# Optimization experiments

Measured on AMD Instinct MI355X. Metric: run time of the kernel, lower is better.

The kernel has to match this reference:

```python
import jax, jax.numpy as jnp
import numpy as np

P = 10      # num_prototypes == embed_dim
H = 2       # num_heads
F = 64      # ffn_dim
L = 2       # transformer_blocks
DH = P // H # head dim = 5


def _layernorm(x, g, b, eps=1e-5):
    mu = jnp.mean(x, axis=-1, keepdims=True)
    var = jnp.var(x, axis=-1, keepdims=True)
    return (x - mu) * jax.lax.rsqrt(var + eps) * g + b


def setup_inputs() -> dict:
    key = jax.random.key(0)
    ks = jax.random.split(key, 16)
    B = 1_000_000
    inp = {
        "x": jax.random.normal(ks[0], (B, 8), dtype=jnp.float32),
        "prototypes": jax.random.normal(ks[1], (P, 8), dtype=jnp.float32),
        # attention projections, stacked over layers
        "Wq": jax.random.normal(ks[2], (L, P, P), dtype=jnp.float32) * 0.1,
        "bq": jnp.zeros((L, P), dtype=jnp.float32),
        "Wk": jax.random.normal(ks[3], (L, P, P), dtype=jnp.float32) * 0.1,
        "bk": jnp.zeros((L, P), dtype=jnp.float32),
        "Wv": jax.random.normal(ks[4], (L, P, P), dtype=jnp.float32) * 0.1,
        "bv": jnp.zeros((L, P), dtype=jnp.float32),
        "Wo": jax.random.normal(ks[5], (L, P, P), dtype=jnp.float32) * 0.1,
        "bo": jnp.zeros((L, P), dtype=jnp.float32),
        "ln1_g": jnp.ones((L, P), dtype=jnp.float32),
        "ln1_b": jnp.zeros((L, P), dtype=jnp.float32),
        "ln2_g": jnp.ones((L, P), dtype=jnp.float32),
        "ln2_b": jnp.zeros((L, P), dtype=jnp.float32),
        # FFN
        "W1": jax.random.normal(ks[6], (L, P, F), dtype=jnp.float32) * 0.1,
        "b1": jnp.zeros((L, F), dtype=jnp.float32),
        "W2": jax.random.normal(ks[7], (L, F, P), dtype=jnp.float32) * 0.1,
        "b2": jnp.zeros((L, P), dtype=jnp.float32),
        # classifier (num_classes=2 -> single logit + sigmoid)
        "Wc": jax.random.normal(ks[8], (P, 1), dtype=jnp.float32) * 0.1,
        "bc": jnp.zeros((1,), dtype=jnp.float32),
    }
    return inp


def _forward(x, prototypes, Wq, bq, Wk, bk, Wv, bv, Wo, bo,
             ln1_g, ln1_b, ln2_g, ln2_b, W1, b1, W2, b2, Wc, bc):
    # ---- vectorized RBF kernel matrix (replaces the B*P python loop) ----
    x2 = jnp.sum(x * x, axis=-1, keepdims=True)            # [B,1]
    p2 = jnp.sum(prototypes * prototypes, axis=-1)          # [P]
    sq = x2 + p2[None, :] - 2.0 * (x @ prototypes.T)        # [B,P]
    km = jnp.exp(-sq)                                       # [B,P] quantum-kernel proxy

    seq = km[:, None, :]                                    # [B, S=1, P]
    scale = 1.0 / jnp.sqrt(jnp.asarray(DH, dtype=seq.dtype))
    B = seq.shape[0]

    for l in range(L):  # small fixed layer count
        # pre-norm multi-head self-attention (seq_len == 1)
        h = _layernorm(seq, ln1_g[l], ln1_b[l])
        q = (h @ Wq[l] + bq[l]).reshape(B, 1, H, DH)
        k = (h @ Wk[l] + bk[l]).reshape(B, 1, H, DH)
        v = (h @ Wv[l] + bv[l]).reshape(B, 1, H, DH)
        scores = jnp.einsum('bqhd,bkhd->bhqk', q, k) * scale
        attn = jax.nn.softmax(scores, axis=-1)
        o = jnp.einsum('bhqk,bkhd->bqhd', attn, v).reshape(B, 1, P)
        seq = seq + (o @ Wo[l] + bo[l])
        # pre-norm FFN
        h2 = _layernorm(seq, ln2_g[l], ln2_b[l])
        seq = seq + (jax.nn.gelu(h2 @ W1[l] + b1[l]) @ W2[l] + b2[l])

    logits = seq[:, 0, :] @ Wc + bc                          # [B,1]
    return jax.nn.sigmoid(logits)


def reference(x, prototypes, Wq, bq, Wk, bk, Wv, bv, Wo, bo,
              ln1_g, ln1_b, ln2_g, ln2_b, W1, b1, W2, b2, Wc, bc):
    return _forward(x, prototypes, Wq, bq, Wk, bk, Wv, bv, Wo, bo,
                    ln1_g, ln1_b, ln2_g, ln2_b, W1, b1, W2, b2, Wc, bc)
```

## Files before the change

kernel.cpp:

```cpp
#include <hip/hip_runtime.h>
#include <cmath>

#define PP 10
#define FF 64
#define BLOCK 256
#define NG 8
#define EPB ((BLOCK / 64) * NG * 16)
#define L2E 1.44269504088896f

typedef float f32x4 __attribute__((ext_vector_type(4)));
typedef _Float16 f16x4 __attribute__((ext_vector_type(4)));
typedef _Float16 h2 __attribute__((ext_vector_type(2)));

struct GeluCoef { float c[5]; };

#define NFRAG 19
#define FB_B2 (NFRAG * 128)
#define F_HC  (FB_B2 + 256)

__device__ __forceinline__ float fast_sigmoid(float z) {
    return __builtin_amdgcn_rcpf(1.0f + exp2f(-L2E * z));
}

__device__ __forceinline__ unsigned int pack_h2f(float a, float b) {
    _Float16 ha = (_Float16)a, hb = (_Float16)b;
    unsigned short ua = __builtin_bit_cast(unsigned short, ha);
    unsigned short ub = __builtin_bit_cast(unsigned short, hb);
    return (unsigned int)ua | ((unsigned int)ub << 16);
}

__device__ __forceinline__ h2 h2bcast(float v) {
    _Float16 h = (_Float16)v;
    h2 r; r.x = h; r.y = h; return r;
}

#define MFMA(a, b, c) __builtin_amdgcn_mfma_f32_16x16x16f16((a), (b), (c), 0, 0, 0)

__global__ __launch_bounds__(256) void prep2(
    const float* __restrict__ Wv, const float* __restrict__ bv,
    const float* __restrict__ Wo, const float* __restrict__ bo,
    const float* __restrict__ ln1g, const float* __restrict__ ln1b,
    const float* __restrict__ ln2g, const float* __restrict__ ln2b,
    const float* __restrict__ W1, const float* __restrict__ b1,
    const float* __restrict__ W2, const float* __restrict__ b2,
    const float* __restrict__ Wc, const float* __restrict__ bc,
    float* __restrict__ ws)
{
    const int t = threadIdx.x;
    unsigned int* wsu = (unsigned int*)ws;

    for (int idx = t; idx < NFRAG * 128; idx += 256) {
        int F = idx >> 7, d = idx & 127;
        int ln = d >> 1, half = d & 1;
        int row = ln & 15;
        int k0 = 4 * (ln >> 4) + 2 * half;
        float v[2] = {0.0f, 0.0f};
        if (F < 2) {
            int l = F;
            if (row < PP) {
                for (int kk = 0; kk < 2; ++kk) {
                    int j = k0 + kk;
                    if (j < PP) {
                        float s = 0.0f;
                        for (int m = 0; m < PP; ++m)
                            s += Wv[l*PP*PP + j*PP + m] * Wo[l*PP*PP + m*PP + row];
                        v[kk] = ln1g[l*PP + j] * s;
                    } else if (j == PP) {
                        float s = bo[l*PP + row];
                        for (int m = 0; m < PP; ++m)
                            s += bv[l*PP + m] * Wo[l*PP*PP + m*PP + row];
                        for (int jj = 0; jj < PP; ++jj) {
                            float ww = 0.0f;
                            for (int m = 0; m < PP; ++m)
                                ww += Wv[l*PP*PP + jj*PP + m] * Wo[l*PP*PP + m*PP + row];
                            s += ln1b[l*PP + jj] * ww;
                        }
                        v[kk] = s;
                    }
                }
            }
        } else if (F < 10) {
            int l = (F - 2) >> 2, m = (F - 2) & 3;
            int f = 16 * m + row;
            for (int kk = 0; kk < 2; ++kk) {
                int j = k0 + kk;
                if (j < PP) {
                    v[kk] = ln2g[l*PP + j] * W1[l*PP*FF + j*FF + f];
                } else if (j == PP) {
                    float s = b1[l*FF + f];
                    for (int jj = 0; jj < PP; ++jj)
                        s += ln2b[l*PP + jj] * W1[l*PP*FF + jj*FF + f];
                    v[kk] = s;
                }
            }
        } else if (F < 14) {
            int c = F - 10;
            if (row < PP) {
                for (int kk = 0; kk < 2; ++kk) {
                    int f = 16 * c + k0 + kk;
                    v[kk] = W2[f*PP + row];
                }
            }
        } else if (F < 18) {
            int c = F - 14;
            if (row == 0) {
                for (int kk = 0; kk < 2; ++kk) {
                    int f = 16 * c + k0 + kk;
                    float s = 0.0f;
                    for (int o = 0; o < PP; ++o) s += W2[FF*PP + f*PP + o] * Wc[o];
                    v[kk] = s;
                }
            }
        } else {
            if (row == 0) {
                for (int kk = 0; kk < 2; ++kk) {
                    int k = k0 + kk;
                    if (k < PP) v[kk] = Wc[k];
                }
            }
        }
        wsu[idx] = pack_h2f(v[0], v[1]);
    }

    if (t < 256) {
        int ln = t >> 2, rr = t & 3;
        int o = 4 * (ln >> 4) + rr;
        ws[FB_B2 + t] = (o < PP) ? b2[o] : 0.0f;
    }
    if (t == 0) {
        float s = bc[0];
        for (int o = 0; o < PP; ++o) s += Wc[o] * b2[PP + o];
        ws[F_HC] = s;
    }
}


__device__ __forceinline__ f16x4 ln_pack(f32x4 s, int q) {
    float ls = (s.x + s.y) + (s.z + s.w);
    float lq = fmaf(s.x, s.x, fmaf(s.y, s.y, fmaf(s.z, s.z, s.w * s.w)));
    ls += __shfl_xor(ls, 16); ls += __shfl_xor(ls, 32);
    lq += __shfl_xor(lq, 16); lq += __shfl_xor(lq, 32);
    float mu = ls * 0.1f;
    float var = fmaf(-mu, mu, lq * 0.1f);
    float rs = __builtin_amdgcn_rsqf(var + 1e-5f);
    float mrs = -mu * rs;
    uint2 u;
    u.x = pack_h2f(fmaf(s.x, rs, mrs), fmaf(s.y, rs, mrs));
    u.y = (q == 2) ? 0x00003C00u
                   : pack_h2f(fmaf(s.z, rs, mrs), fmaf(s.w, rs, mrs));
    return __builtin_bit_cast(f16x4, u);
}

__device__ __forceinline__ f16x4 gelu_pack(f32x4 tv, h2 G0, h2 G1, h2 G2, h2 G3,
                                           h2 G4, h2 HLF) {
    h2 X0 = __builtin_bit_cast(h2, pack_h2f(tv.x, tv.y));
    h2 X1 = __builtin_bit_cast(h2, pack_h2f(tv.z, tv.w));
    h2 S0 = X0 * X0, S1 = X1 * X1;
    h2 P0 = S0 * G4 + G3, P1 = S1 * G4 + G3;
    P0 = S0 * P0 + G2; P1 = S1 * P1 + G2;
    P0 = S0 * P0 + G1; P1 = S1 * P1 + G1;
    P0 = S0 * P0 + G0; P1 = S1 * P1 + G0;
    h2 H0 = X0 * P0 + HLF, H1 = X1 * P1 + HLF;
    h2 U0 = X0 * H0, U1 = X1 * H1;
    uint2 u;
    u.x = __builtin_bit_cast(unsigned int, U0);
    u.y = __builtin_bit_cast(unsigned int, U1);
    return __builtin_bit_cast(f16x4, u);
}

__global__ __launch_bounds__(BLOCK, 2) void hq_mfma(
    const float* __restrict__ x, const float* __restrict__ protos,
    const float* __restrict__ ws, float* __restrict__ out, int B, GeluCoef gc)
{
    const int t = threadIdx.x;
    const int lane = t & 63;
    const int q = lane >> 4;
    const int col = lane & 15;
    const int wbase = blockIdx.x * EPB + (t >> 6) * (NG * 16);

    const uint2* fr = (const uint2*)ws;
    f16x4 aattn[2], affn1[2][4], affn2[4], aw2c[4], ahead;
#pragma unroll
    for (int l = 0; l < 2; ++l)
        aattn[l] = __builtin_bit_cast(f16x4, fr[l * 64 + lane]);
#pragma unroll
    for (int l = 0; l < 2; ++l)
#pragma unroll
        for (int m = 0; m < 4; ++m)
            affn1[l][m] = __builtin_bit_cast(f16x4, fr[(2 + l * 4 + m) * 64 + lane]);
#pragma unroll
    for (int c = 0; c < 4; ++c)
        affn2[c] = __builtin_bit_cast(f16x4, fr[(10 + c) * 64 + lane]);
#pragma unroll
    for (int c = 0; c < 4; ++c)
        aw2c[c] = __builtin_bit_cast(f16x4, fr[(14 + c) * 64 + lane]);
    ahead = __builtin_bit_cast(f16x4, fr[18 * 64 + lane]);

    const f32x4* wv4 = (const f32x4*)ws;
    f32x4 b2f = wv4[FB_B2 / 4 + lane];
    float hc = ws[F_HC];
    f32x4 zero4 = {0.0f, 0.0f, 0.0f, 0.0f};
    f32x4 zi = zero4;
    if (lane < 16) zi.x = hc;

    const float4* p4 = (const float4*)protos;
    float4 pa[4], pb[4];
    float mp2[4];
#pragma unroll
    for (int r = 0; r < 4; ++r) {
        int p = 4 * q + r;
        int pc = (p < PP) ? p : 0;
        pa[r] = p4[pc * 2]; pb[r] = p4[pc * 2 + 1];
        float s2 = pa[r].x*pa[r].x + pa[r].y*pa[r].y + pa[r].z*pa[r].z + pa[r].w*pa[r].w
                 + pb[r].x*pb[r].x + pb[r].y*pb[r].y + pb[r].z*pb[r].z + pb[r].w*pb[r].w;
        mp2[r] = (p < PP) ? (-L2E * s2) : -1e30f;
    }

    const float4* x4 = (const float4*)x;
    f32x4 seq[NG];
#pragma unroll
    for (int g = 0; g < NG; ++g) {
        int e = wbase + g * 16 + col;
        if (e >= B) e = B - 1;
        float4 xa = x4[e * 2], xb = x4[e * 2 + 1];
        float x2 = xa.x*xa.x + xa.y*xa.y + xa.z*xa.z + xa.w*xa.w
                 + xb.x*xb.x + xb.y*xb.y + xb.z*xb.z + xb.w*xb.w;
#pragma unroll
        for (int r = 0; r < 4; ++r) {
            float dot = xa.x*pa[r].x + xa.y*pa[r].y + xa.z*pa[r].z + xa.w*pa[r].w
                      + xb.x*pb[r].x + xb.y*pb[r].y + xb.z*pb[r].z + xb.w*pb[r].w;
            float s = fmaf(2.0f * L2E, dot, fmaf(-L2E, x2, mp2[r]));
            seq[g][r] = exp2f(s);
        }
    }

    const h2 GC0 = h2bcast(gc.c[0]);
    const h2 GC1 = h2bcast(gc.c[1]);
    const h2 GC2 = h2bcast(gc.c[2]);
    const h2 GC3 = h2bcast(gc.c[3]);
    const h2 GC4 = h2bcast(gc.c[4]);
    const h2 HLF = h2bcast(0.5f);

    f16x4 y[NG];

#pragma unroll
    for (int g = 0; g < NG; ++g) y[g] = ln_pack(seq[g], q);
#pragma unroll
    for (int g = 0; g < NG; ++g) seq[g] = MFMA(aattn[0], y[g], seq[g]);
#pragma unroll
    for (int g = 0; g < NG; ++g) y[g] = ln_pack(seq[g], q);
#pragma unroll
    for (int g = 0; g < NG; ++g) {
        f32x4 t0 = MFMA(affn1[0][0], y[g], zero4);
        f32x4 t1 = MFMA(affn1[0][1], y[g], zero4);
        f32x4 t2 = MFMA(affn1[0][2], y[g], zero4);
        f32x4 t3 = MFMA(affn1[0][3], y[g], zero4);
        f16x4 u0 = gelu_pack(t0, GC0, GC1, GC2, GC3, GC4, HLF);
        f16x4 u1 = gelu_pack(t1, GC0, GC1, GC2, GC3, GC4, HLF);
        f16x4 u2 = gelu_pack(t2, GC0, GC1, GC2, GC3, GC4, HLF);
        f16x4 u3 = gelu_pack(t3, GC0, GC1, GC2, GC3, GC4, HLF);
        f32x4 o = MFMA(affn2[0], u0, seq[g]);
        o = MFMA(affn2[1], u1, o);
        o = MFMA(affn2[2], u2, o);
        o = MFMA(affn2[3], u3, o);
        seq[g] = o + b2f;
    }

#pragma unroll
    for (int g = 0; g < NG; ++g) y[g] = ln_pack(seq[g], q);
#pragma unroll
    for (int g = 0; g < NG; ++g) seq[g] = MFMA(aattn[1], y[g], seq[g]);
#pragma unroll
    for (int g = 0; g < NG; ++g) y[g] = ln_pack(seq[g], q);
#pragma unroll
    for (int g = 0; g < NG; ++g) {
        f32x4 t0 = MFMA(affn1[1][0], y[g], zero4);
        f32x4 t1 = MFMA(affn1[1][1], y[g], zero4);
        f32x4 t2 = MFMA(affn1[1][2], y[g], zero4);
        f32x4 t3 = MFMA(affn1[1][3], y[g], zero4);
        f16x4 u0 = gelu_pack(t0, GC0, GC1, GC2, GC3, GC4, HLF);
        f16x4 u1 = gelu_pack(t1, GC0, GC1, GC2, GC3, GC4, HLF);
        f16x4 u2 = gelu_pack(t2, GC0, GC1, GC2, GC3, GC4, HLF);
        f16x4 u3 = gelu_pack(t3, GC0, GC1, GC2, GC3, GC4, HLF);
        f32x4 zc = MFMA(aw2c[0], u0, zi);
        zc = MFMA(aw2c[1], u1, zc);
        zc = MFMA(aw2c[2], u2, zc);
        zc = MFMA(aw2c[3], u3, zc);
        uint2 sh;
        sh.x = pack_h2f(seq[g].x, seq[g].y);
        sh.y = pack_h2f(seq[g].z, seq[g].w);
        zc = MFMA(ahead, __builtin_bit_cast(f16x4, sh), zc);
        float r = fast_sigmoid(zc.x);
        int e0 = wbase + g * 16 + col;
        if (q == 0 && e0 < B) out[e0] = r;
    }
}

extern "C" void kernel_launch(void* const* d_in, const int* in_sizes, int n_in,
                              void* d_out, int out_size, void* d_ws, size_t ws_size,
                              hipStream_t stream) {
    const float* x      = (const float*)d_in[0];
    const float* protos = (const float*)d_in[1];
    const float* Wv   = (const float*)d_in[6];
    const float* bv   = (const float*)d_in[7];
    const float* Wo   = (const float*)d_in[8];
    const float* bo   = (const float*)d_in[9];
    const float* ln1g = (const float*)d_in[10];
    const float* ln1b = (const float*)d_in[11];
    const float* ln2g = (const float*)d_in[12];
    const float* ln2b = (const float*)d_in[13];
    const float* W1   = (const float*)d_in[14];
    const float* b1   = (const float*)d_in[15];
    const float* W2   = (const float*)d_in[16];
    const float* b2   = (const float*)d_in[17];
    const float* Wc   = (const float*)d_in[18];
    const float* bc   = (const float*)d_in[19];
    float* out = (float*)d_out;
    float* ws  = (float*)d_ws;

    GeluCoef gcoef;
    {
        const double PI = 3.14159265358979323846;
        const double cc = 0.7978845608028654, aa = 0.044715;
        double sv[5], gd[5];
        for (int k = 0; k < 5; ++k) {
            double tk = 1.85 + 1.85 * std::cos((2 * k + 1) * PI / 10.0);
            sv[k] = tk * tk;
            gd[k] = std::tanh(cc * (tk + aa * tk * tk * tk)) / tk;
        }
        for (int j = 1; j < 5; ++j)
            for (int i = 4; i >= j; --i)
                gd[i] = (gd[i] - gd[i - 1]) / (sv[i] - sv[i - j]);
        double c[5] = {0, 0, 0, 0, 0};
        c[0] = gd[4];
        for (int k = 3; k >= 0; --k) {
            for (int i = 4; i >= 1; --i) c[i] = c[i - 1] - sv[k] * c[i];
            c[0] = -sv[k] * c[0] + gd[k];
        }
        for (int i = 0; i < 5; ++i) gcoef.c[i] = (float)(0.5 * c[i]);
    }

    prep2<<<1, 256, 0, stream>>>(Wv, bv, Wo, bo, ln1g, ln1b, ln2g, ln2b,
                                 W1, b1, W2, b2, Wc, bc, ws);

    const int B = in_sizes[0] / 8;
    const int grid = (B + EPB - 1) / EPB;
    hq_mfma<<<grid, BLOCK, 0, stream>>>(x, protos, ws, out, B, gcoef);
}
```

Before: 155.3 us.

## Parallelize weight prep over blocks, use pkrtz conversions, fold RBF scale into prototypes

Runs the weight-preparation kernel on 8 blocks with a grid-stride loop, so the single-block prep no longer sits serially ahead of the main kernel. Replaces the manual float-to-half packing with the hardware cvt_pkrtz instruction, which rounds toward zero and may slightly change numerics. Pre-scales the prototypes by 2*log2(e) so the RBF exponent becomes a plain FMA chain. Adds a full-block fast path that uses strided x loads and stores without bounds checks.

```diff
diff --git a/kernel.cpp b/kernel.cpp
--- a/kernel.cpp
+++ b/kernel.cpp
@@ -6,6 +6,7 @@
 #define BLOCK 256
 #define NG 8
 #define EPB ((BLOCK / 64) * NG * 16)
+#define PGRID 8
 #define L2E 1.44269504088896f
 
 typedef float f32x4 __attribute__((ext_vector_type(4)));
@@ -27,6 +28,10 @@
     unsigned short ua = __builtin_bit_cast(unsigned short, ha);
     unsigned short ub = __builtin_bit_cast(unsigned short, hb);
     return (unsigned int)ua | ((unsigned int)ub << 16);
+}
+
+__device__ __forceinline__ unsigned int pkrtz(float a, float b) {
+    return __builtin_bit_cast(unsigned int, __builtin_amdgcn_cvt_pkrtz(a, b));
 }
 
 __device__ __forceinline__ h2 h2bcast(float v) {
@@ -46,10 +51,11 @@
     const float* __restrict__ Wc, const float* __restrict__ bc,
     float* __restrict__ ws)
 {
-    const int t = threadIdx.x;
+    const int gt = blockIdx.x * 256 + threadIdx.x;
+    const int GSZ = 256 * PGRID;
     unsigned int* wsu = (unsigned int*)ws;
 
-    for (int idx = t; idx < NFRAG * 128; idx += 256) {
+    for (int idx = gt; idx < NFRAG * 128; idx += GSZ) {
         int F = idx >> 7, d = idx & 127;
         int ln = d >> 1, half = d & 1;
         int row = ln & 15;
@@ -122,12 +128,12 @@
         wsu[idx] = pack_h2f(v[0], v[1]);
     }
 
-    if (t < 256) {
-        int ln = t >> 2, rr = t & 3;
+    for (int idx = gt; idx < 256; idx += GSZ) {
+        int ln = idx >> 2, rr = idx & 3;
         int o = 4 * (ln >> 4) + rr;
-        ws[FB_B2 + t] = (o < PP) ? b2[o] : 0.0f;
-    }
-    if (t == 0) {
+        ws[FB_B2 + idx] = (o < PP) ? b2[o] : 0.0f;
+    }
+    if (gt == 0) {
         float s = bc[0];
         for (int o = 0; o < PP; ++o) s += Wc[o] * b2[PP + o];
         ws[F_HC] = s;
@@ -145,16 +151,16 @@
     float rs = __builtin_amdgcn_rsqf(var + 1e-5f);
     float mrs = -mu * rs;
     uint2 u;
-    u.x = pack_h2f(fmaf(s.x, rs, mrs), fmaf(s.y, rs, mrs));
-    u.y = (q == 2) ? 0x00003C00u
-                   : pack_h2f(fmaf(s.z, rs, mrs), fmaf(s.w, rs, mrs));
+    u.x = pkrtz(fmaf(s.x, rs, mrs), fmaf(s.y, rs, mrs));
+    unsigned int hi = pkrtz(fmaf(s.z, rs, mrs), fmaf(s.w, rs, mrs));
+    u.y = (q == 2) ? 0x00003C00u : hi;
     return __builtin_bit_cast(f16x4, u);
 }
 
 __device__ __forceinline__ f16x4 gelu_pack(f32x4 tv, h2 G0, h2 G1, h2 G2, h2 G3,
                                            h2 G4, h2 HLF) {
-    h2 X0 = __builtin_bit_cast(h2, pack_h2f(tv.x, tv.y));
-    h2 X1 = __builtin_bit_cast(h2, pack_h2f(tv.z, tv.w));
+    h2 X0 = __builtin_bit_cast(h2, pkrtz(tv.x, tv.y));
+    h2 X1 = __builtin_bit_cast(h2, pkrtz(tv.z, tv.w));
     h2 S0 = X0 * X0, S1 = X1 * X1;
     h2 P0 = S0 * G4 + G3, P1 = S1 * G4 + G3;
     P0 = S0 * P0 + G2; P1 = S1 * P1 + G2;
@@ -168,6 +174,23 @@
     return __builtin_bit_cast(f16x4, u);
 }
 
+__device__ __forceinline__ void feat4(f32x4* sg, float4 xa, float4 xb,
+                                      const float4* pa, const float4* pb,
+                                      const float* mp2) {
+    float x2 = xa.x*xa.x + xa.y*xa.y + xa.z*xa.z + xa.w*xa.w
+             + xb.x*xb.x + xb.y*xb.y + xb.z*xb.z + xb.w*xb.w;
+    float xc = -L2E * x2;
+#pragma unroll
+    for (int r = 0; r < 4; ++r) {
+        float s = xc + mp2[r];
+        s = fmaf(xa.x, pa[r].x, s); s = fmaf(xa.y, pa[r].y, s);
+        s = fmaf(xa.z, pa[r].z, s); s = fmaf(xa.w, pa[r].w, s);
+        s = fmaf(xb.x, pb[r].x, s); s = fmaf(xb.y, pb[r].y, s);
+        s = fmaf(xb.z, pb[r].z, s); s = fmaf(xb.w, pb[r].w, s);
+        (*sg)[r] = exp2f(s);
+    }
+}
+
 __global__ __launch_bounds__(BLOCK, 2) void hq_mfma(
     const float* __restrict__ x, const float* __restrict__ protos,
     const float* __restrict__ ws, float* __restrict__ out, int B, GeluCoef gc)
@@ -177,6 +200,7 @@
     const int q = lane >> 4;
     const int col = lane & 15;
     const int wbase = blockIdx.x * EPB + (t >> 6) * (NG * 16);
+    const bool fullblk = (wbase + NG * 16) <= B;
 
     const uint2* fr = (const uint2*)ws;
     f16x4 aattn[2], affn1[2][4], affn2[4], aw2c[4], ahead;
@@ -210,27 +234,28 @@
     for (int r = 0; r < 4; ++r) {
         int p = 4 * q + r;
         int pc = (p < PP) ? p : 0;
-        pa[r] = p4[pc * 2]; pb[r] = p4[pc * 2 + 1];
-        float s2 = pa[r].x*pa[r].x + pa[r].y*pa[r].y + pa[r].z*pa[r].z + pa[r].w*pa[r].w
-                 + pb[r].x*pb[r].x + pb[r].y*pb[r].y + pb[r].z*pb[r].z + pb[r].w*pb[r].w;
+        float4 a = p4[pc * 2], b = p4[pc * 2 + 1];
+        float s2 = a.x*a.x + a.y*a.y + a.z*a.z + a.w*a.w
+                 + b.x*b.x + b.y*b.y + b.z*b.z + b.w*b.w;
         mp2[r] = (p < PP) ? (-L2E * s2) : -1e30f;
+        const float TW = 2.0f * L2E;
+        pa[r].x = TW*a.x; pa[r].y = TW*a.y; pa[r].z = TW*a.z; pa[r].w = TW*a.w;
+        pb[r].x = TW*b.x; pb[r].y = TW*b.y; pb[r].z = TW*b.z; pb[r].w = TW*b.w;
     }
 
     const float4* x4 = (const float4*)x;
     f32x4 seq[NG];
-#pragma unroll
-    for (int g = 0; g < NG; ++g) {
-        int e = wbase + g * 16 + col;
-        if (e >= B) e = B - 1;
-        float4 xa = x4[e * 2], xb = x4[e * 2 + 1];
-        float x2 = xa.x*xa.x + xa.y*xa.y + xa.z*xa.z + xa.w*xa.w
-                 + xb.x*xb.x + xb.y*xb.y + xb.z*xb.z + xb.w*xb.w;
-#pragma unroll
-        for (int r = 0; r < 4; ++r) {
-            float dot = xa.x*pa[r].x + xa.y*pa[r].y + xa.z*pa[r].z + xa.w*pa[r].w
-                      + xb.x*pb[r].x + xb.y*pb[r].y + xb.z*pb[r].z + xb.w*pb[r].w;
-            float s = fmaf(2.0f * L2E, dot, fmaf(-L2E, x2, mp2[r]));
-            seq[g][r] = exp2f(s);
+    if (fullblk) {
+        const float4* xb4 = x4 + 2 * (size_t)(wbase + col);
+#pragma unroll
+        for (int g = 0; g < NG; ++g)
+            feat4(&seq[g], xb4[32 * g], xb4[32 * g + 1], pa, pb, mp2);
+    } else {
+#pragma unroll
+        for (int g = 0; g < NG; ++g) {
+            int e = wbase + g * 16 + col;
+            if (e >= B) e = B - 1;
+            feat4(&seq[g], x4[e * 2], x4[e * 2 + 1], pa, pb, mp2);
         }
     }
 
@@ -287,12 +312,15 @@
         zc = MFMA(aw2c[2], u2, zc);
         zc = MFMA(aw2c[3], u3, zc);
         uint2 sh;
-        sh.x = pack_h2f(seq[g].x, seq[g].y);
-        sh.y = pack_h2f(seq[g].z, seq[g].w);
+        sh.x = pkrtz(seq[g].x, seq[g].y);
+        sh.y = pkrtz(seq[g].z, seq[g].w);
         zc = MFMA(ahead, __builtin_bit_cast(f16x4, sh), zc);
         float r = fast_sigmoid(zc.x);
-        int e0 = wbase + g * 16 + col;
-        if (q == 0 && e0 < B) out[e0] = r;
+        if (q == 0) {
+            int e0 = wbase + g * 16 + col;
+            if (fullblk) out[e0] = r;
+            else if (e0 < B) out[e0] = r;
+        }
     }
 }
 
@@ -340,8 +368,8 @@
         for (int i = 0; i < 5; ++i) gcoef.c[i] = (float)(0.5 * c[i]);
     }
 
-    prep2<<<1, 256, 0, stream>>>(Wv, bv, Wo, bo, ln1g, ln1b, ln2g, ln2b,
-                                 W1, b1, W2, b2, Wc, bc, ws);
+    prep2<<<PGRID, 256, 0, stream>>>(Wv, bv, Wo, bo, ln1g, ln1b, ln2g, ln2b,
+                                     W1, b1, W2, b2, Wc, bc, ws);
 
     const int B = in_sizes[0] / 8;
     const int grid = (B + EPB - 1) / EPB;
```

Result: faster. 151.1 us (-2.7%).
